# Optimization experiments

Hardware: AMD Instinct MI355X
Metric: run time of the kernel (lower is better)

## Reference

```python
import jax, jax.numpy as jnp
import numpy as np

NUM_FEATS = 40
FEAT_EMB_DIM = 16
MARK_DIM = 1024
HIDDEN = 4096
BATCH = 16384


def setup_inputs() -> dict:
    key = jax.random.key(0)
    ks = jax.random.split(key, 9)
    in_dim = NUM_FEATS * FEAT_EMB_DIM + 2 * MARK_DIM
    return {
        "emb_i": jax.random.normal(ks[0], (BATCH, MARK_DIM), dtype=jnp.float32),
        "emb_a": jax.random.normal(ks[1], (BATCH, MARK_DIM), dtype=jnp.float32),
        "feat_mask": jax.random.randint(ks[2], (BATCH, NUM_FEATS), 0, 2, dtype=jnp.int32),
        "feat_on_embs": jax.random.normal(ks[3], (NUM_FEATS, FEAT_EMB_DIM), dtype=jnp.float32),
        "feat_off_embs": jax.random.normal(ks[4], (NUM_FEATS, FEAT_EMB_DIM), dtype=jnp.float32),
        "W1": jax.random.normal(ks[5], (HIDDEN, in_dim), dtype=jnp.float32) / np.sqrt(in_dim),
        "b1": jax.random.normal(ks[6], (HIDDEN,), dtype=jnp.float32) * 0.01,
        "W2": jax.random.normal(ks[7], (1, HIDDEN), dtype=jnp.float32) / np.sqrt(HIDDEN),
        "b2": jax.random.normal(ks[8], (1,), dtype=jnp.float32) * 0.01,
    }


def reference(emb_i, emb_a, feat_mask, feat_on_embs, feat_off_embs, W1, b1, W2, b2):
    # Per-feature embedding select: index == position, so on/off tables broadcast
    # over batch; mask picks on-emb where feature is positive. [B, F, E]
    feats = jnp.where(feat_mask[:, :, None] > 0,
                      feat_on_embs[None, :, :],
                      feat_off_embs[None, :, :])
    B = emb_i.shape[0]
    concat = jnp.concatenate(
        [emb_i, emb_a, feats.reshape(B, -1)], axis=-1)  # [B, 2*D + F*E]
    h = jax.nn.relu(concat @ W1.T + b1)                 # [B, HIDDEN]
    return h @ W2.T + b2                                # [B, 1]
```

## Files before the change

kernel.cpp:

```cpp
#include <hip/hip_runtime.h>
#include <hip/hip_bf16.h>
#include <stdint.h>

#define BATCH 16384
#define MARK  1024
#define NF    40
#define FE    16
#define KDIM  2688
#define HID   4096
#define BK    64
#define NKT   (KDIM / BK)

typedef __bf16 bf16x8 __attribute__((ext_vector_type(8)));
typedef float  f32x4  __attribute__((ext_vector_type(4)));

static __device__ __forceinline__ unsigned short f2bf(float f) {
  union { float f; uint32_t u; } v; v.f = f;
  uint32_t u = v.u;
  uint32_t r = (u + 0x7FFFu + ((u >> 16) & 1u)) >> 16;
  return (unsigned short)r;
}

__global__ __launch_bounds__(256) void build_concat(
    const float* __restrict__ emb_i, const float* __restrict__ emb_a,
    const int* __restrict__ mask, const float* __restrict__ fon,
    const float* __restrict__ foff, unsigned short* __restrict__ out) {
  const int b = blockIdx.x;
  const float4* ri = (const float4*)(emb_i + (size_t)b * MARK);
  const float4* ra = (const float4*)(emb_a + (size_t)b * MARK);
  const int* mrow = mask + b * NF;
  unsigned short* orow = out + (size_t)b * KDIM;
  for (int g = threadIdx.x; g < KDIM / 4; g += 256) {
    const int base = g * 4;
    float4 v;
    if (base < MARK) {
      v = ri[g];
    } else if (base < 2 * MARK) {
      v = ra[g - MARK / 4];
    } else {
      const int idx = base - 2 * MARK;
      const int f = idx >> 4;
      const float* tab = (mrow[f] > 0) ? fon : foff;
      v = *(const float4*)(tab + f * FE + (idx & 15));
    }
    ushort4 o;
    o.x = f2bf(v.x); o.y = f2bf(v.y); o.z = f2bf(v.z); o.w = f2bf(v.w);
    *(ushort4*)(orow + base) = o;
  }
}

__global__ __launch_bounds__(256) void convert_w1(
    const float* __restrict__ w, unsigned short* __restrict__ o, int n4) {
  const int stride = gridDim.x * 256;
  for (int i = blockIdx.x * 256 + threadIdx.x; i < n4; i += stride) {
    float4 v = ((const float4*)w)[i];
    ushort4 u;
    u.x = f2bf(v.x); u.y = f2bf(v.y); u.z = f2bf(v.z); u.w = f2bf(v.w);
    ((ushort4*)o)[i] = u;
  }
}

__global__ __launch_bounds__(256) void out_init(float* __restrict__ out,
                                                const float* __restrict__ b2) {
  const int i = blockIdx.x * 256 + threadIdx.x;
  if (i < BATCH) out[i] = b2[0];
}

#define GL16(g, l)                                                              \
  __builtin_amdgcn_global_load_lds(                                             \
      (const __attribute__((address_space(1))) void*)(g),                       \
      (__attribute__((address_space(3))) void*)(l), 16, 0, 0)

#define BAR()        __builtin_amdgcn_s_barrier()
#define WAIT_LGKM0() asm volatile("s_waitcnt lgkmcnt(0)" ::: "memory")
#define WAIT_VM6()   asm volatile("s_waitcnt vmcnt(6)" ::: "memory")

__global__ __launch_bounds__(512, 2) void gemm_fused(
    const unsigned short* __restrict__ A,
    const unsigned short* __restrict__ Wb,
    const float* __restrict__ b1,
    const float* __restrict__ w2,
    float* __restrict__ out) {
  __shared__ unsigned short sA[2][256 * BK];
  __shared__ unsigned short sB[2][256 * BK];
  __shared__ float spart[2][4][128];

  const int tid  = threadIdx.x;
  const int wid  = tid >> 6;
  const int lane = tid & 63;
  const int fr   = lane & 15;
  const int k8   = lane >> 4;
  const int wm   = wid >> 2;
  const int wn   = wid & 3;

  const int bid = blockIdx.x;
  const int xcd = bid & 7;
  const int j   = bid >> 3;
  const int sub = j >> 5;
  const int sm  = (j >> 2) & 7;
  const int sn  = j & 3;
  const int tile_m = (xcd >> 1) * 16 + (sub >> 1) * 8 + sm;
  const int tile_n = (xcd & 1) * 8 + (sub & 1) * 4 + sn;

  const int lrow = lane >> 3;
  const int lsrc = ((lane & 7) ^ lrow) * 8;
  const unsigned short* Aptr =
      A + ((size_t)tile_m * 256 + lrow) * KDIM + lsrc;
  const unsigned short* Bptr =
      Wb + ((size_t)tile_n * 256 + lrow) * KDIM + lsrc;

  const int swz0 = ((k8 ^ (fr & 7)) * 8);
  const int swz1 = (((4 + k8) ^ (fr & 7)) * 8);

#define STAGEA(BUF, MH, KT)                                                    \
  { _Pragma("unroll") for (int g = 0; g < 2; ++g) {                            \
      const int r0 = g * 128 + (MH)*64 + wid * 8;                              \
      GL16(Aptr + (size_t)r0 * KDIM + (KT)*BK, &sA[BUF][r0 * BK]); } }

#define STAGEB(BUF, NH, KT)                                                    \
  { _Pragma("unroll") for (int g = 0; g < 2; ++g) {                            \
      const int r0 = g * 128 + (wid >> 2) * 64 + (NH)*32 + (wid & 3) * 8;      \
      GL16(Bptr + (size_t)r0 * KDIM + (KT)*BK, &sB[BUF][r0 * BK]); } }

#define LOADA(BUF, MH)                                                         \
  { _Pragma("unroll") for (int i = 0; i < 4; ++i) {                            \
      const unsigned short* p =                                                \
          &sA[BUF][(wm * 128 + (MH)*64 + i * 16 + fr) * BK];                   \
      af[i][0] = *(const bf16x8*)(p + swz0);                                   \
      af[i][1] = *(const bf16x8*)(p + swz1); } }

#define LOADB(BUF, NH)                                                         \
  { _Pragma("unroll") for (int j = 0; j < 2; ++j) {                            \
      const unsigned short* p =                                                \
          &sB[BUF][(wn * 64 + (NH)*32 + j * 16 + fr) * BK];                    \
      bfr[j][0] = *(const bf16x8*)(p + swz0);                                  \
      bfr[j][1] = *(const bf16x8*)(p + swz1); } }

#define MMA(MH, NH)                                                            \
  { __builtin_amdgcn_s_setprio(1);                                             \
    _Pragma("unroll") for (int i = 0; i < 4; ++i)                              \
    _Pragma("unroll") for (int j = 0; j < 2; ++j) {                            \
      acc[(MH)*4 + i][(NH)*2 + j] = __builtin_amdgcn_mfma_f32_16x16x32_bf16(   \
          af[i][0], bfr[j][0], acc[(MH)*4 + i][(NH)*2 + j], 0, 0, 0);          \
      acc[(MH)*4 + i][(NH)*2 + j] = __builtin_amdgcn_mfma_f32_16x16x32_bf16(   \
          af[i][1], bfr[j][1], acc[(MH)*4 + i][(NH)*2 + j], 0, 0, 0); }        \
    __builtin_amdgcn_s_setprio(0); }

  f32x4 acc[8][4];
#pragma unroll
  for (int i = 0; i < 8; ++i)
#pragma unroll
    for (int j = 0; j < 4; ++j) acc[i][j] = (f32x4){0.f, 0.f, 0.f, 0.f};
  bf16x8 af[4][2], bfr[2][2];

  float b1v[4], w2v[4];
  const int gcol = tile_n * 256 + wn * 64 + fr;
#pragma unroll
  for (int jj = 0; jj < 4; ++jj) {
    b1v[jj] = b1[gcol + jj * 16];
    w2v[jj] = w2[gcol + jj * 16];
  }

  STAGEA(0, 0, 0); STAGEB(0, 1, 0); STAGEA(0, 1, 0); STAGEB(0, 0, 0);
  STAGEA(1, 0, 1); STAGEB(1, 1, 1); STAGEA(1, 1, 1);
  WAIT_VM6();
  BAR();

#pragma unroll 1
  for (int t = 0; t < NKT; t += 2) {
    int t2 = t + 2; if (t2 >= NKT) t2 -= NKT;
    int t3 = t + 3; if (t3 >= NKT) t3 -= NKT;
    LOADA(0, 0); LOADB(0, 0);
    STAGEB(1, 0, t + 1);
    BAR(); WAIT_LGKM0();
    MMA(0, 0);
    BAR();
    LOADB(0, 1);
    STAGEA(0, 0, t2);
    BAR(); WAIT_LGKM0();
    MMA(0, 1);
    BAR();
    LOADA(0, 1);
    STAGEB(0, 1, t2);
    BAR(); WAIT_LGKM0();
    MMA(1, 1);
    BAR();
    LOADB(0, 0);
    STAGEA(0, 1, t2);
    BAR(); WAIT_LGKM0();
    MMA(1, 0);
    WAIT_VM6();
    BAR();
    LOADA(1, 0); LOADB(1, 0);
    STAGEB(0, 0, t2);
    BAR(); WAIT_LGKM0();
    MMA(0, 0);
    BAR();
    LOADB(1, 1);
    STAGEA(1, 0, t3);
    BAR(); WAIT_LGKM0();
    MMA(0, 1);
    BAR();
    LOADA(1, 1);
    STAGEB(1, 1, t3);
    BAR(); WAIT_LGKM0();
    MMA(1, 1);
    BAR();
    LOADB(1, 0);
    STAGEA(1, 1, t3);
    BAR(); WAIT_LGKM0();
    MMA(1, 0);
    WAIT_VM6();
    BAR();
  }

#pragma unroll
  for (int i = 0; i < 8; ++i) {
    float vs[4];
#pragma unroll
    for (int r = 0; r < 4; ++r) {
      float s = 0.f;
#pragma unroll
      for (int jj = 0; jj < 4; ++jj) {
        float h = acc[i][jj][r] + b1v[jj];
        h = h > 0.f ? h : 0.f;
        s = fmaf(h, w2v[jj], s);
      }
      vs[r] = s;
    }
#pragma unroll
    for (int r = 0; r < 4; ++r) {
      vs[r] += __shfl_xor(vs[r], 1, 16);
      vs[r] += __shfl_xor(vs[r], 2, 16);
      vs[r] += __shfl_xor(vs[r], 4, 16);
      vs[r] += __shfl_xor(vs[r], 8, 16);
    }
    if (fr == 0) {
#pragma unroll
      for (int r = 0; r < 4; ++r)
        spart[wm][wn][i * 16 + k8 * 4 + r] = vs[r];
    }
  }
  __syncthreads();
  if (tid < 256) {
    const int rl = tid & 127, wmr = tid >> 7;
    float s = spart[wmr][0][rl] + spart[wmr][1][rl] +
              spart[wmr][2][rl] + spart[wmr][3][rl];
    atomicAdd(&out[(size_t)tile_m * 256 + tid], s);
  }
}

extern "C" void kernel_launch(void* const* d_in, const int* in_sizes, int n_in,
                              void* d_out, int out_size, void* d_ws, size_t ws_size,
                              hipStream_t stream) {
  const float* emb_i = (const float*)d_in[0];
  const float* emb_a = (const float*)d_in[1];
  const int*   fmask = (const int*)d_in[2];
  const float* fon   = (const float*)d_in[3];
  const float* foff  = (const float*)d_in[4];
  const float* W1    = (const float*)d_in[5];
  const float* b1    = (const float*)d_in[6];
  const float* W2    = (const float*)d_in[7];
  const float* b2    = (const float*)d_in[8];
  float* out = (float*)d_out;

  unsigned short* concat = (unsigned short*)d_ws;
  unsigned short* w1b    = concat + (size_t)BATCH * KDIM;

  build_concat<<<BATCH, 256, 0, stream>>>(emb_i, emb_a, fmask, fon, foff, concat);
  convert_w1<<<2048, 256, 0, stream>>>(W1, w1b, HID * KDIM / 4);
  out_init<<<BATCH / 256, 256, 0, stream>>>(out, b2);
  gemm_fused<<<(BATCH / 256) * (HID / 256), 512, 0, stream>>>(concat, w1b, b1,
                                                              W2, out);
}
```

Baseline: 540.6 us.

## Switch GEMM to 32x32x16 MFMA tiles with fewer LDS phases per k-step

Replaces the 16x16x32 bf16 MFMA fragments with 32x32x16 MFMA, changing the LDS fragment layout and swizzle offsets, the accumulator shape, and the epilogue reduction. The k-loop schedule is reorganized into two MMA phases per buffer instead of four, with staging of A and B tiles regrouped accordingly, reducing barriers and LDS reads per FLOP. This risks different register pressure with 16-wide accumulators and changed global-load interleaving relative to the vmcnt waits.

```diff
diff --git a/kernel.cpp b/kernel.cpp
--- a/kernel.cpp
+++ b/kernel.cpp
@@ -12,7 +12,7 @@
 #define NKT   (KDIM / BK)
 
 typedef __bf16 bf16x8 __attribute__((ext_vector_type(8)));
-typedef float  f32x4  __attribute__((ext_vector_type(4)));
+typedef float  f32x16 __attribute__((ext_vector_type(16)));
 
 static __device__ __forceinline__ unsigned short f2bf(float f) {
   union { float f; uint32_t u; } v; v.f = f;
@@ -88,8 +88,8 @@
   const int tid  = threadIdx.x;
   const int wid  = tid >> 6;
   const int lane = tid & 63;
-  const int fr   = lane & 15;
-  const int k8   = lane >> 4;
+  const int l31  = lane & 31;
+  const int hi   = lane >> 5;
   const int wm   = wid >> 2;
   const int wn   = wid & 3;
 
@@ -109,60 +109,63 @@
   const unsigned short* Bptr =
       Wb + ((size_t)tile_n * 256 + lrow) * KDIM + lsrc;
 
-  const int swz0 = ((k8 ^ (fr & 7)) * 8);
-  const int swz1 = (((4 + k8) ^ (fr & 7)) * 8);
-
-#define STAGEA(BUF, MH, KT)                                                    \
-  { _Pragma("unroll") for (int g = 0; g < 2; ++g) {                            \
-      const int r0 = g * 128 + (MH)*64 + wid * 8;                              \
-      GL16(Aptr + (size_t)r0 * KDIM + (KT)*BK, &sA[BUF][r0 * BK]); } }
-
-#define STAGEB(BUF, NH, KT)                                                    \
-  { _Pragma("unroll") for (int g = 0; g < 2; ++g) {                            \
-      const int r0 = g * 128 + (wid >> 2) * 64 + (NH)*32 + (wid & 3) * 8;      \
-      GL16(Bptr + (size_t)r0 * KDIM + (KT)*BK, &sB[BUF][r0 * BK]); } }
+  int cko[4];
+#pragma unroll
+  for (int k_ = 0; k_ < 4; ++k_)
+    cko[k_] = (((2 * k_ + hi) ^ (lane & 7)) * 8);
+
+#define STAGEA(BUF, U, KT)                                                     \
+  { _Pragma("unroll") for (int g_ = 0; g_ < 2; ++g_) {                         \
+      const int r0 = (U)*128 + g_ * 64 + wid * 8;                              \
+      GL16(Aptr + (size_t)r0 * KDIM + (size_t)(KT)*BK, &sA[BUF][r0 * BK]); } }
+
+#define STAGEB(BUF, U, KT)                                                     \
+  { _Pragma("unroll") for (int g_ = 0; g_ < 2; ++g_) {                         \
+      const int r0 = (U)*128 + g_ * 64 + wid * 8;                              \
+      GL16(Bptr + (size_t)r0 * KDIM + (size_t)(KT)*BK, &sB[BUF][r0 * BK]); } }
 
 #define LOADA(BUF, MH)                                                         \
-  { _Pragma("unroll") for (int i = 0; i < 4; ++i) {                            \
+  { _Pragma("unroll") for (int mt_ = 0; mt_ < 2; ++mt_) {                      \
       const unsigned short* p =                                                \
-          &sA[BUF][(wm * 128 + (MH)*64 + i * 16 + fr) * BK];                   \
-      af[i][0] = *(const bf16x8*)(p + swz0);                                   \
-      af[i][1] = *(const bf16x8*)(p + swz1); } }
-
-#define LOADB(BUF, NH)                                                         \
-  { _Pragma("unroll") for (int j = 0; j < 2; ++j) {                            \
+          &sA[BUF][(wm * 128 + (MH)*64 + mt_ * 32 + l31) * BK];                \
+      _Pragma("unroll") for (int k_ = 0; k_ < 4; ++k_)                         \
+          af[mt_][k_] = *(const bf16x8*)(p + cko[k_]); } }
+
+#define LOADB(BUF)                                                             \
+  { _Pragma("unroll") for (int nt_ = 0; nt_ < 2; ++nt_) {                      \
       const unsigned short* p =                                                \
-          &sB[BUF][(wn * 64 + (NH)*32 + j * 16 + fr) * BK];                    \
-      bfr[j][0] = *(const bf16x8*)(p + swz0);                                  \
-      bfr[j][1] = *(const bf16x8*)(p + swz1); } }
-
-#define MMA(MH, NH)                                                            \
+          &sB[BUF][(wn * 64 + nt_ * 32 + l31) * BK];                           \
+      _Pragma("unroll") for (int k_ = 0; k_ < 4; ++k_)                         \
+          bfr[nt_][k_] = *(const bf16x8*)(p + cko[k_]); } }
+
+#define MMA(MH)                                                                \
   { __builtin_amdgcn_s_setprio(1);                                             \
-    _Pragma("unroll") for (int i = 0; i < 4; ++i)                              \
-    _Pragma("unroll") for (int j = 0; j < 2; ++j) {                            \
-      acc[(MH)*4 + i][(NH)*2 + j] = __builtin_amdgcn_mfma_f32_16x16x32_bf16(   \
-          af[i][0], bfr[j][0], acc[(MH)*4 + i][(NH)*2 + j], 0, 0, 0);          \
-      acc[(MH)*4 + i][(NH)*2 + j] = __builtin_amdgcn_mfma_f32_16x16x32_bf16(   \
-          af[i][1], bfr[j][1], acc[(MH)*4 + i][(NH)*2 + j], 0, 0, 0); }        \
+    _Pragma("unroll") for (int k_ = 0; k_ < 4; ++k_)                           \
+    _Pragma("unroll") for (int mt_ = 0; mt_ < 2; ++mt_)                        \
+    _Pragma("unroll") for (int nt_ = 0; nt_ < 2; ++nt_)                        \
+      acc[(MH)*2 + mt_][nt_] = __builtin_amdgcn_mfma_f32_32x32x16_bf16(        \
+          af[mt_][k_], bfr[nt_][k_], acc[(MH)*2 + mt_][nt_], 0, 0, 0);         \
     __builtin_amdgcn_s_setprio(0); }
 
-  f32x4 acc[8][4];
-#pragma unroll
-  for (int i = 0; i < 8; ++i)
-#pragma unroll
-    for (int j = 0; j < 4; ++j) acc[i][j] = (f32x4){0.f, 0.f, 0.f, 0.f};
-  bf16x8 af[4][2], bfr[2][2];
-
-  float b1v[4], w2v[4];
-  const int gcol = tile_n * 256 + wn * 64 + fr;
-#pragma unroll
-  for (int jj = 0; jj < 4; ++jj) {
-    b1v[jj] = b1[gcol + jj * 16];
-    w2v[jj] = w2[gcol + jj * 16];
-  }
-
-  STAGEA(0, 0, 0); STAGEB(0, 1, 0); STAGEA(0, 1, 0); STAGEB(0, 0, 0);
-  STAGEA(1, 0, 1); STAGEB(1, 1, 1); STAGEA(1, 1, 1);
+  f32x16 acc[4][2];
+#pragma unroll
+  for (int i = 0; i < 4; ++i)
+#pragma unroll
+    for (int n_ = 0; n_ < 2; ++n_)
+#pragma unroll
+      for (int r_ = 0; r_ < 16; ++r_) acc[i][n_][r_] = 0.f;
+  bf16x8 af[2][4], bfr[2][4];
+
+  float b1v[2], w2v[2];
+#pragma unroll
+  for (int nt_ = 0; nt_ < 2; ++nt_) {
+    const int col = tile_n * 256 + wn * 64 + nt_ * 32 + l31;
+    b1v[nt_] = b1[col];
+    w2v[nt_] = w2[col];
+  }
+
+  STAGEA(0, 0, 0); STAGEB(0, 0, 0); STAGEB(0, 1, 0); STAGEA(0, 1, 0);
+  STAGEA(1, 0, 1); STAGEB(1, 0, 1); STAGEB(1, 1, 1);
   WAIT_VM6();
   BAR();
 
@@ -170,75 +173,46 @@
   for (int t = 0; t < NKT; t += 2) {
     int t2 = t + 2; if (t2 >= NKT) t2 -= NKT;
     int t3 = t + 3; if (t3 >= NKT) t3 -= NKT;
-    LOADA(0, 0); LOADB(0, 0);
-    STAGEB(1, 0, t + 1);
-    BAR(); WAIT_LGKM0();
-    MMA(0, 0);
-    BAR();
-    LOADB(0, 1);
-    STAGEA(0, 0, t2);
-    BAR(); WAIT_LGKM0();
-    MMA(0, 1);
+    LOADA(0, 0); LOADB(0);
+    STAGEA(1, 1, t + 1);
+    BAR(); WAIT_LGKM0();
+    MMA(0);
     BAR();
     LOADA(0, 1);
-    STAGEB(0, 1, t2);
-    BAR(); WAIT_LGKM0();
-    MMA(1, 1);
-    BAR();
-    LOADB(0, 0);
+    STAGEA(0, 0, t2); STAGEB(0, 0, t2); STAGEB(0, 1, t2);
+    BAR(); WAIT_LGKM0();
+    MMA(1);
+    WAIT_VM6();
+    BAR();
+    LOADA(1, 0); LOADB(1);
     STAGEA(0, 1, t2);
     BAR(); WAIT_LGKM0();
-    MMA(1, 0);
+    MMA(0);
+    BAR();
+    LOADA(1, 1);
+    STAGEB(1, 0, t3); STAGEB(1, 1, t3); STAGEA(1, 0, t3);
+    BAR(); WAIT_LGKM0();
+    MMA(1);
     WAIT_VM6();
     BAR();
-    LOADA(1, 0); LOADB(1, 0);
-    STAGEB(0, 0, t2);
-    BAR(); WAIT_LGKM0();
-    MMA(0, 0);
-    BAR();
-    LOADB(1, 1);
-    STAGEA(1, 0, t3);
-    BAR(); WAIT_LGKM0();
-    MMA(0, 1);
-    BAR();
-    LOADA(1, 1);
-    STAGEB(1, 1, t3);
-    BAR(); WAIT_LGKM0();
-    MMA(1, 1);
-    BAR();
-    LOADB(1, 0);
-    STAGEA(1, 1, t3);
-    BAR(); WAIT_LGKM0();
-    MMA(1, 0);
-    WAIT_VM6();
-    BAR();
-  }
-
-#pragma unroll
-  for (int i = 0; i < 8; ++i) {
-    float vs[4];
-#pragma unroll
-    for (int r = 0; r < 4; ++r) {
-      float s = 0.f;
-#pragma unroll
-      for (int jj = 0; jj < 4; ++jj) {
-        float h = acc[i][jj][r] + b1v[jj];
-        h = h > 0.f ? h : 0.f;
-        s = fmaf(h, w2v[jj], s);
-      }
-      vs[r] = s;
-    }
-#pragma unroll
-    for (int r = 0; r < 4; ++r) {
-      vs[r] += __shfl_xor(vs[r], 1, 16);
-      vs[r] += __shfl_xor(vs[r], 2, 16);
-      vs[r] += __shfl_xor(vs[r], 4, 16);
-      vs[r] += __shfl_xor(vs[r], 8, 16);
-    }
-    if (fr == 0) {
-#pragma unroll
-      for (int r = 0; r < 4; ++r)
-        spart[wm][wn][i * 16 + k8 * 4 + r] = vs[r];
+  }
+
+#pragma unroll
+  for (int mt4 = 0; mt4 < 4; ++mt4) {
+#pragma unroll
+    for (int r_ = 0; r_ < 16; ++r_) {
+      float h0 = acc[mt4][0][r_] + b1v[0];
+      float h1 = acc[mt4][1][r_] + b1v[1];
+      h0 = h0 > 0.f ? h0 : 0.f;
+      h1 = h1 > 0.f ? h1 : 0.f;
+      float s = fmaf(h0, w2v[0], h1 * w2v[1]);
+      s += __shfl_xor(s, 1, 32);
+      s += __shfl_xor(s, 2, 32);
+      s += __shfl_xor(s, 4, 32);
+      s += __shfl_xor(s, 8, 32);
+      s += __shfl_xor(s, 16, 32);
+      if (l31 == 0)
+        spart[wm][wn][mt4 * 32 + (r_ & 3) + 8 * (r_ >> 2) + 4 * hi] = s;
     }
   }
   __syncthreads();
```

After: 556.4 us. 1.03x slower.

## Double-buffer MFMA operand registers to overlap LDS reads with matrix math

Applied to the files above, without the earlier changes.

Splits the A and B register fragments into two alternating sets so the next quadrant's LDS reads are issued before the current quadrant's MFMAs. The explicit lgkmcnt(0) waits are removed and the compiler is left to insert them, and the vmcnt wait moves earlier (vmcnt 4) ahead of the next buffer's loads. Launch bounds change from 2 blocks per CU to 1 so the extra registers fit. This trades occupancy for a deeper software pipeline inside each wave, which risks less latency hiding across blocks and possible ordering hazards now that the global-to-LDS stage order has changed.

```diff
diff --git a/kernel.cpp b/kernel.cpp
--- a/kernel.cpp
+++ b/kernel.cpp
@@ -71,11 +71,11 @@
       (const __attribute__((address_space(1))) void*)(g),                       \
       (__attribute__((address_space(3))) void*)(l), 16, 0, 0)
 
-#define BAR()        __builtin_amdgcn_s_barrier()
-#define WAIT_LGKM0() asm volatile("s_waitcnt lgkmcnt(0)" ::: "memory")
-#define WAIT_VM6()   asm volatile("s_waitcnt vmcnt(6)" ::: "memory")
-
-__global__ __launch_bounds__(512, 2) void gemm_fused(
+#define BAR()      __builtin_amdgcn_s_barrier()
+#define WAIT_VM6() asm volatile("s_waitcnt vmcnt(6)" ::: "memory")
+#define WAIT_VM4() asm volatile("s_waitcnt vmcnt(4)" ::: "memory")
+
+__global__ __launch_bounds__(512, 1) void gemm_fused(
     const unsigned short* __restrict__ A,
     const unsigned short* __restrict__ Wb,
     const float* __restrict__ b1,
@@ -115,43 +115,43 @@
 #define STAGEA(BUF, MH, KT)                                                    \
   { _Pragma("unroll") for (int g = 0; g < 2; ++g) {                            \
       const int r0 = g * 128 + (MH)*64 + wid * 8;                              \
-      GL16(Aptr + (size_t)r0 * KDIM + (KT)*BK, &sA[BUF][r0 * BK]); } }
+      GL16(Aptr + (size_t)r0 * KDIM + (size_t)(KT)*BK, &sA[BUF][r0 * BK]); } }
 
 #define STAGEB(BUF, NH, KT)                                                    \
   { _Pragma("unroll") for (int g = 0; g < 2; ++g) {                            \
       const int r0 = g * 128 + (wid >> 2) * 64 + (NH)*32 + (wid & 3) * 8;      \
-      GL16(Bptr + (size_t)r0 * KDIM + (KT)*BK, &sB[BUF][r0 * BK]); } }
-
-#define LOADA(BUF, MH)                                                         \
+      GL16(Bptr + (size_t)r0 * KDIM + (size_t)(KT)*BK, &sB[BUF][r0 * BK]); } }
+
+#define LOADA_TO(DST, BUF, MH)                                                 \
   { _Pragma("unroll") for (int i = 0; i < 4; ++i) {                            \
       const unsigned short* p =                                                \
           &sA[BUF][(wm * 128 + (MH)*64 + i * 16 + fr) * BK];                   \
-      af[i][0] = *(const bf16x8*)(p + swz0);                                   \
-      af[i][1] = *(const bf16x8*)(p + swz1); } }
-
-#define LOADB(BUF, NH)                                                         \
-  { _Pragma("unroll") for (int j = 0; j < 2; ++j) {                            \
+      DST[i][0] = *(const bf16x8*)(p + swz0);                                  \
+      DST[i][1] = *(const bf16x8*)(p + swz1); } }
+
+#define LOADB_TO(DST, BUF, NH)                                                 \
+  { _Pragma("unroll") for (int jj = 0; jj < 2; ++jj) {                         \
       const unsigned short* p =                                                \
-          &sB[BUF][(wn * 64 + (NH)*32 + j * 16 + fr) * BK];                    \
-      bfr[j][0] = *(const bf16x8*)(p + swz0);                                  \
-      bfr[j][1] = *(const bf16x8*)(p + swz1); } }
-
-#define MMA(MH, NH)                                                            \
+          &sB[BUF][(wn * 64 + (NH)*32 + jj * 16 + fr) * BK];                   \
+      DST[jj][0] = *(const bf16x8*)(p + swz0);                                 \
+      DST[jj][1] = *(const bf16x8*)(p + swz1); } }
+
+#define MMA_Q(ASET, BSET, MH, NH)                                              \
   { __builtin_amdgcn_s_setprio(1);                                             \
     _Pragma("unroll") for (int i = 0; i < 4; ++i)                              \
-    _Pragma("unroll") for (int j = 0; j < 2; ++j) {                            \
-      acc[(MH)*4 + i][(NH)*2 + j] = __builtin_amdgcn_mfma_f32_16x16x32_bf16(   \
-          af[i][0], bfr[j][0], acc[(MH)*4 + i][(NH)*2 + j], 0, 0, 0);          \
-      acc[(MH)*4 + i][(NH)*2 + j] = __builtin_amdgcn_mfma_f32_16x16x32_bf16(   \
-          af[i][1], bfr[j][1], acc[(MH)*4 + i][(NH)*2 + j], 0, 0, 0); }        \
+    _Pragma("unroll") for (int jj = 0; jj < 2; ++jj) {                         \
+      acc[(MH)*4 + i][(NH)*2 + jj] = __builtin_amdgcn_mfma_f32_16x16x32_bf16(  \
+          ASET[i][0], BSET[jj][0], acc[(MH)*4 + i][(NH)*2 + jj], 0, 0, 0);     \
+      acc[(MH)*4 + i][(NH)*2 + jj] = __builtin_amdgcn_mfma_f32_16x16x32_bf16(  \
+          ASET[i][1], BSET[jj][1], acc[(MH)*4 + i][(NH)*2 + jj], 0, 0, 0); }   \
     __builtin_amdgcn_s_setprio(0); }
 
   f32x4 acc[8][4];
 #pragma unroll
   for (int i = 0; i < 8; ++i)
 #pragma unroll
-    for (int j = 0; j < 4; ++j) acc[i][j] = (f32x4){0.f, 0.f, 0.f, 0.f};
-  bf16x8 af[4][2], bfr[2][2];
+    for (int jj = 0; jj < 4; ++jj) acc[i][jj] = (f32x4){0.f, 0.f, 0.f, 0.f};
+  bf16x8 aX[4][2], aY[4][2], bX[2][2], bY[2][2];
 
   float b1v[4], w2v[4];
   const int gcol = tile_n * 256 + wn * 64 + fr;
@@ -161,56 +161,57 @@
     w2v[jj] = w2[gcol + jj * 16];
   }
 
-  STAGEA(0, 0, 0); STAGEB(0, 1, 0); STAGEA(0, 1, 0); STAGEB(0, 0, 0);
+  STAGEA(0, 0, 0); STAGEB(0, 0, 0); STAGEB(0, 1, 0); STAGEA(0, 1, 0);
   STAGEA(1, 0, 1); STAGEB(1, 1, 1); STAGEA(1, 1, 1);
   WAIT_VM6();
   BAR();
+  LOADA_TO(aX, 0, 0); LOADB_TO(bX, 0, 0);
 
 #pragma unroll 1
   for (int t = 0; t < NKT; t += 2) {
     int t2 = t + 2; if (t2 >= NKT) t2 -= NKT;
     int t3 = t + 3; if (t3 >= NKT) t3 -= NKT;
-    LOADA(0, 0); LOADB(0, 0);
     STAGEB(1, 0, t + 1);
-    BAR(); WAIT_LGKM0();
-    MMA(0, 0);
-    BAR();
-    LOADB(0, 1);
+    LOADB_TO(bY, 0, 1);
+    BAR();
+    MMA_Q(aX, bX, 0, 0);
+    BAR();
     STAGEA(0, 0, t2);
-    BAR(); WAIT_LGKM0();
-    MMA(0, 1);
-    BAR();
-    LOADA(0, 1);
+    LOADA_TO(aY, 0, 1);
+    BAR();
+    MMA_Q(aX, bY, 0, 1);
+    BAR();
     STAGEB(0, 1, t2);
-    BAR(); WAIT_LGKM0();
-    MMA(1, 1);
-    BAR();
-    LOADB(0, 0);
+    LOADB_TO(bX, 0, 0);
+    BAR();
+    MMA_Q(aY, bY, 1, 1);
+    BAR();
+    WAIT_VM4();
+    LOADA_TO(aX, 1, 0); LOADB_TO(bY, 1, 0);
     STAGEA(0, 1, t2);
-    BAR(); WAIT_LGKM0();
-    MMA(1, 0);
-    WAIT_VM6();
-    BAR();
-    LOADA(1, 0); LOADB(1, 0);
+    BAR();
+    MMA_Q(aY, bX, 1, 0);
+    BAR();
     STAGEB(0, 0, t2);
-    BAR(); WAIT_LGKM0();
-    MMA(0, 0);
-    BAR();
-    LOADB(1, 1);
+    LOADB_TO(bX, 1, 1);
+    BAR();
+    MMA_Q(aX, bY, 0, 0);
+    BAR();
     STAGEA(1, 0, t3);
-    BAR(); WAIT_LGKM0();
-    MMA(0, 1);
-    BAR();
-    LOADA(1, 1);
+    LOADA_TO(aY, 1, 1);
+    BAR();
+    MMA_Q(aX, bX, 0, 1);
+    BAR();
     STAGEB(1, 1, t3);
-    BAR(); WAIT_LGKM0();
-    MMA(1, 1);
-    BAR();
-    LOADB(1, 0);
+    LOADB_TO(bY, 1, 0);
+    BAR();
+    MMA_Q(aY, bX, 1, 1);
+    BAR();
+    WAIT_VM4();
+    LOADA_TO(aX, 0, 0); LOADB_TO(bX, 0, 0);
     STAGEA(1, 1, t3);
-    BAR(); WAIT_LGKM0();
-    MMA(1, 0);
-    WAIT_VM6();
+    BAR();
+    MMA_Q(aY, bY, 1, 0);
     BAR();
   }
 
```

After: 671.7 us. +24.3%, slower.
